# Performance work log

Hardware: AMD Instinct MI355X
Metric: run time of the kernel (lower is better)

The kernel has to match this reference:

```python
import jax, jax.numpy as jnp
import numpy as np

B, N, D, H, C = 4, 1024, 768, 12, 3
Dh = D // H                      # 64
HID = int(D * 4.0 * (2.0 / 3.0)) # 2048 (SwiGLU hidden)
EPS = 1e-5


def layernorm(x, g, b):
    m = jnp.mean(x, axis=-1, keepdims=True)
    v = jnp.mean(jnp.square(x - m), axis=-1, keepdims=True)
    return (x - m) * jax.lax.rsqrt(v + EPS) * g + b


def setup_inputs() -> dict:
    key = jax.random.key(0)
    ks = jax.random.split(key, 8)
    x = jax.random.normal(ks[0], (B, N, D), jnp.float32)
    coords = jax.random.uniform(ks[1], (B, N, C), jnp.float32)
    qkv_w = jax.random.normal(ks[2], (3 * D, D), jnp.float32) * 0.02
    qkv_b = jnp.zeros((3 * D,), jnp.float32)
    rel_w = jax.random.normal(ks[3], (H, C), jnp.float32) * 0.1
    ln1_g = jnp.ones((D,), jnp.float32)
    ln1_b = jnp.zeros((D,), jnp.float32)
    ln2_g = jnp.ones((D,), jnp.float32)
    ln2_b = jnp.zeros((D,), jnp.float32)
    win_w = jax.random.normal(ks[4], (2 * HID, D), jnp.float32) * 0.02
    win_b = jnp.zeros((2 * HID,), jnp.float32)
    wout_w = jax.random.normal(ks[5], (D, HID), jnp.float32) * 0.02
    wout_b = jnp.zeros((D,), jnp.float32)
    return dict(x=x, coords=coords, ln1_g=ln1_g, ln1_b=ln1_b, qkv_w=qkv_w,
                qkv_b=qkv_b, rel_w=rel_w, ln2_g=ln2_g, ln2_b=ln2_b,
                win_w=win_w, win_b=win_b, wout_w=wout_w, wout_b=wout_b)


def reference(x, coords, ln1_g, ln1_b, qkv_w, qkv_b, rel_w, ln2_g, ln2_b,
              win_w, win_b, wout_w, wout_b):
    # --- PatchAttention on norm1(x) ---
    h = layernorm(x, ln1_g, ln1_b)
    qkv = h @ qkv_w.T + qkv_b                    # (B,N,3D)
    q, k, v = jnp.split(qkv, 3, axis=-1)

    def heads(t):  # (B,N,D) -> (B,H,N,Dh)
        return t.reshape(B, N, H, Dh).transpose(0, 2, 1, 3)

    qh, kh, vh = heads(q), heads(k), heads(v)
    scale = 1.0 / np.sqrt(Dh).astype(np.float32)
    scores = jnp.einsum('bhid,bhjd->bhij', qh, kh) * scale
    # coord bias: (coords_i - coords_j) . W_h  ==  p[b,h,i] - p[b,h,j]
    p = jnp.einsum('bnc,hc->bhn', coords, rel_w)  # (B,H,N)
    scores = scores + p[:, :, :, None] - p[:, :, None, :]
    attn = jax.nn.softmax(scores, axis=-1)
    o = jnp.einsum('bhij,bhjd->bhid', attn, vh)   # (B,H,N,Dh)
    o = o.transpose(0, 2, 1, 3).reshape(B, N, D)
    x = x + o

    # --- SwiGLU FFN on norm2(x) ---
    h2 = layernorm(x, ln2_g, ln2_b)
    uv = h2 @ win_w.T + win_b                     # (B,N,2*HID)
    u, g = jnp.split(uv, 2, axis=-1)
    act = jax.nn.silu(u) * g
    return x + act @ wout_w.T + wout_b
```

## Files before the change

### kernel.cpp

```cpp
#include <hip/hip_runtime.h>
#include <math.h>

typedef unsigned short u16;
typedef __bf16 bf16x8 __attribute__((ext_vector_type(8)));
typedef __bf16 bf16x4 __attribute__((ext_vector_type(4)));
typedef u16 u16x4 __attribute__((ext_vector_type(4)));
typedef float f32x4 __attribute__((ext_vector_type(4)));

#define NTOK 1024
#define DMODEL 768
#define NHEAD 12
#define LD3 2304
#define HIDDIM 2048

__device__ __forceinline__ float b2f(u16 u) {
  unsigned int t = ((unsigned int)u) << 16;
  float f;
  __builtin_memcpy(&f, &t, 4);
  return f;
}
__device__ __forceinline__ u16 f2b(float f) {
  unsigned int t;
  __builtin_memcpy(&t, &f, 4);
  t += 0x7fffu + ((t >> 16) & 1u);
  return (u16)(t >> 16);
}

__device__ __forceinline__ void gl_lds16(const u16* g, u16* l) {
  __builtin_amdgcn_global_load_lds(
      (__attribute__((address_space(1))) const unsigned int*)g,
      (__attribute__((address_space(3))) unsigned int*)l, 16, 0, 0);
}

__global__ __launch_bounds__(256) void signal_kernel(float* __restrict__ out,
                                                     int n, float c) {
  int i = blockIdx.x * 256 + threadIdx.x;
  if (i < n) out[i] = c;
}

struct CanonJobs {
  const void* s[13];
  u16* d[13];
  int n[13];
};

__global__ __launch_bounds__(256) void canon_kernel(CanonJobs jobs) {
  __shared__ int csh;
  u16 v = ((const u16*)jobs.s[0])[2 * threadIdx.x];
  int e = (v >> 7) & 0xFF;
  unsigned long long m = __ballot(e >= 0xC0);
  if (threadIdx.x == 0) csh = 0;
  __syncthreads();
  if ((threadIdx.x & 63) == 0) atomicAdd(&csh, __popcll(m));
  __syncthreads();
  bool isf32 = csh >= 8;

  int j = blockIdx.y;
  int n4 = jobs.n[j] >> 2;
  const void* s = jobs.s[j];
  u16* d = jobs.d[j];
  for (int i = blockIdx.x * 256 + threadIdx.x; i < n4; i += gridDim.x * 256) {
    if (isf32) {
      f32x4 vv = *((const f32x4*)s + i);
      u16x4 o = {f2b(vv[0]), f2b(vv[1]), f2b(vv[2]), f2b(vv[3])};
      *((u16x4*)d + i) = o;
    } else {
      *((u16x4*)d + i) = *((const u16x4*)s + i);
    }
  }
}

__global__ __launch_bounds__(256) void ln_bf16_kernel(
    const u16* __restrict__ x, const u16* __restrict__ g,
    const u16* __restrict__ b, u16* __restrict__ out) {
  int row = blockIdx.x;
  int tid = threadIdx.x;
  const u16* xr = x + (size_t)row * DMODEL;
  float v0 = b2f(xr[tid]), v1 = b2f(xr[tid + 256]), v2 = b2f(xr[tid + 512]);
  float s = v0 + v1 + v2;
  float q = v0 * v0 + v1 * v1 + v2 * v2;
#pragma unroll
  for (int off = 32; off; off >>= 1) {
    s += __shfl_xor(s, off, 64);
    q += __shfl_xor(q, off, 64);
  }
  __shared__ float rs[4], rq[4];
  int wv = tid >> 6;
  if ((tid & 63) == 0) { rs[wv] = s; rq[wv] = q; }
  __syncthreads();
  s = rs[0] + rs[1] + rs[2] + rs[3];
  q = rq[0] + rq[1] + rq[2] + rq[3];
  float mean = s * (1.0f / 768.0f);
  float var = q * (1.0f / 768.0f) - mean * mean;
  float inv = rsqrtf(var + 1e-5f);
  u16* outr = out + (size_t)row * DMODEL;
  outr[tid]       = f2b((v0 - mean) * inv * b2f(g[tid])       + b2f(b[tid]));
  outr[tid + 256] = f2b((v1 - mean) * inv * b2f(g[tid + 256]) + b2f(b[tid + 256]));
  outr[tid + 512] = f2b((v2 - mean) * inv * b2f(g[tid + 512]) + b2f(b[tid + 512]));
}

__global__ __launch_bounds__(256) void ln_f32_kernel(
    const float* __restrict__ x, const u16* __restrict__ g,
    const u16* __restrict__ b, u16* __restrict__ out) {
  int row = blockIdx.x;
  int tid = threadIdx.x;
  const float* xr = x + (size_t)row * DMODEL;
  float v0 = xr[tid], v1 = xr[tid + 256], v2 = xr[tid + 512];
  float s = v0 + v1 + v2;
  float q = v0 * v0 + v1 * v1 + v2 * v2;
#pragma unroll
  for (int off = 32; off; off >>= 1) {
    s += __shfl_xor(s, off, 64);
    q += __shfl_xor(q, off, 64);
  }
  __shared__ float rs[4], rq[4];
  int wv = tid >> 6;
  if ((tid & 63) == 0) { rs[wv] = s; rq[wv] = q; }
  __syncthreads();
  s = rs[0] + rs[1] + rs[2] + rs[3];
  q = rq[0] + rq[1] + rq[2] + rq[3];
  float mean = s * (1.0f / 768.0f);
  float var = q * (1.0f / 768.0f) - mean * mean;
  float inv = rsqrtf(var + 1e-5f);
  u16* outr = out + (size_t)row * DMODEL;
  outr[tid]       = f2b((v0 - mean) * inv * b2f(g[tid])       + b2f(b[tid]));
  outr[tid + 256] = f2b((v1 - mean) * inv * b2f(g[tid + 256]) + b2f(b[tid + 256]));
  outr[tid + 512] = f2b((v2 - mean) * inv * b2f(g[tid + 512]) + b2f(b[tid + 512]));
}

__global__ __launch_bounds__(256) void gemm_bt(
    const u16* __restrict__ Ap, const u16* __restrict__ Wp,
    const u16* __restrict__ bias, u16* __restrict__ Cp, int Nn, int K) {
  __shared__ __align__(16) u16 Al[3 * 128 * 32], Bl[3 * 64 * 32];
  int lane = threadIdx.x & 63;
  int wv = threadIdx.x >> 6;
  int q16 = lane & 15, quad = lane >> 4;
  int mB0 = blockIdx.y * 128;
  int nB0 = blockIdx.x * 64;
  int mW = (wv >> 1) * 64, nW = (wv & 1) * 32;
  int srow = lane >> 2;
  int scol = ((lane & 3) ^ ((lane >> 3) & 3)) * 8;
  int sx8 = (quad ^ ((q16 >> 1) & 3)) * 8;
  int r0 = wv * 32 + srow, r1 = r0 + 16;
  int rb = wv * 16 + srow;
  const u16* Ag0 = Ap + (size_t)(mB0 + r0) * K + scol;
  const u16* Ag1 = Ap + (size_t)(mB0 + r1) * K + scol;
  const u16* Wg  = Wp + (size_t)(nB0 + rb) * K + scol;
  int ch0 = wv * 1024, ch1 = ch0 + 512, chb = wv * 512;
  int nsteps = K >> 5;
  f32x4 acc[4][2] = {};
#pragma unroll
  for (int tt = 0; tt < 2; ++tt) {
    int k0 = tt * 32;
    gl_lds16(Ag0 + k0, Al + tt * 4096 + ch0);
    gl_lds16(Ag1 + k0, Al + tt * 4096 + ch1);
    gl_lds16(Wg + k0, Bl + tt * 2048 + chb);
  }
  int n3 = nsteps / 3;
  for (int kb = 0; kb < n3; ++kb) {
#pragma unroll
    for (int c = 0; c < 3; ++c) {
      int t = kb * 3 + c;
      if (t < nsteps - 1) asm volatile("s_waitcnt vmcnt(3)" ::: "memory");
      else                asm volatile("s_waitcnt vmcnt(0)" ::: "memory");
      __builtin_amdgcn_sched_barrier(0);
      __builtin_amdgcn_s_barrier();
      __builtin_amdgcn_sched_barrier(0);
      if (t < nsteps - 2) {
        int k0 = (t + 2) * 32;
        int bs = (c + 2) % 3;
        gl_lds16(Ag0 + k0, Al + bs * 4096 + ch0);
        gl_lds16(Ag1 + k0, Al + bs * 4096 + ch1);
        gl_lds16(Wg + k0, Bl + bs * 2048 + chb);
      }
      const __bf16* Ab = (const __bf16*)(Al + c * 4096);
      const __bf16* Bb = (const __bf16*)(Bl + c * 2048);
      bf16x8 af[4], bfr[2];
#pragma unroll
      for (int si = 0; si < 4; ++si)
        af[si] = *(const bf16x8*)(Ab + (mW + si * 16 + q16) * 32 + sx8);
#pragma unroll
      for (int sj = 0; sj < 2; ++sj)
        bfr[sj] = *(const bf16x8*)(Bb + (nW + sj * 16 + q16) * 32 + sx8);
#pragma unroll
      for (int si = 0; si < 4; ++si)
#pragma unroll
        for (int sj = 0; sj < 2; ++sj)
          acc[si][sj] = __builtin_amdgcn_mfma_f32_16x16x32_bf16(af[si], bfr[sj], acc[si][sj], 0, 0, 0);
    }
  }
#pragma unroll
  for (int si = 0; si < 4; ++si)
#pragma unroll
    for (int sj = 0; sj < 2; ++sj) {
      int col = nB0 + nW + sj * 16 + q16;
      float bcol = b2f(bias[col]);
#pragma unroll
      for (int r = 0; r < 4; ++r) {
        int rowi = mB0 + mW + si * 16 + quad * 4 + r;
        Cp[(size_t)rowi * Nn + col] = f2b(acc[si][sj][r] + bcol);
      }
    }
}

__global__ __launch_bounds__(256) void gemm_out_f32(
    const u16* __restrict__ Ap, const u16* __restrict__ Wp,
    const u16* __restrict__ bias, const float* __restrict__ res,
    float* __restrict__ out) {
  __shared__ __align__(16) u16 Al[2 * 4096], Bl[2 * 4096];
  int lane = threadIdx.x & 63;
  int wv = threadIdx.x >> 6;
  int q16 = lane & 15, quad = lane >> 4;
  int mB0 = blockIdx.y * 64;
  int nB0 = blockIdx.x * 64;
  int mW = (wv >> 1) * 32, nW = (wv & 1) * 32;
  int lr = lane >> 3, ls = lane & 7;
  int sg = (ls ^ lr) * 8;
  int sx0 = (quad ^ (q16 & 7)) * 8;
  int sx1 = ((4 | quad) ^ (q16 & 7)) * 8;
  const u16* Ag = Ap + (size_t)(mB0 + wv * 16 + lr) * 2048 + sg;
  const u16* Wg = Wp + (size_t)(nB0 + wv * 16 + lr) * 2048 + sg;
  int ch = wv * 1024;
  f32x4 acc[2][2] = {};
#pragma unroll
  for (int i = 0; i < 2; ++i) {
    gl_lds16(Ag + (size_t)i * 8 * 2048, Al + ch + i * 512);
    gl_lds16(Wg + (size_t)i * 8 * 2048, Bl + ch + i * 512);
  }
  for (int kb = 0; kb < 16; ++kb) {
#pragma unroll
    for (int c = 0; c < 2; ++c) {
      int t = kb * 2 + c;
      asm volatile("s_waitcnt vmcnt(0)" ::: "memory");
      __builtin_amdgcn_sched_barrier(0);
      __builtin_amdgcn_s_barrier();
      __builtin_amdgcn_sched_barrier(0);
      if (t < 31) {
        int k0 = (t + 1) * 64;
        int bs = c ^ 1;
#pragma unroll
        for (int i = 0; i < 2; ++i) {
          gl_lds16(Ag + (size_t)i * 8 * 2048 + k0, Al + bs * 4096 + ch + i * 512);
          gl_lds16(Wg + (size_t)i * 8 * 2048 + k0, Bl + bs * 4096 + ch + i * 512);
        }
      }
      const __bf16* Ab = (const __bf16*)(Al + c * 4096);
      const __bf16* Bb = (const __bf16*)(Bl + c * 4096);
      bf16x8 a0[2], a1[2], b0[2], b1[2];
#pragma unroll
      for (int si = 0; si < 2; ++si) {
        a0[si] = *(const bf16x8*)(Ab + (mW + si * 16 + q16) * 64 + sx0);
        a1[si] = *(const bf16x8*)(Ab + (mW + si * 16 + q16) * 64 + sx1);
      }
#pragma unroll
      for (int sj = 0; sj < 2; ++sj) {
        b0[sj] = *(const bf16x8*)(Bb + (nW + sj * 16 + q16) * 64 + sx0);
        b1[sj] = *(const bf16x8*)(Bb + (nW + sj * 16 + q16) * 64 + sx1);
      }
#pragma unroll
      for (int si = 0; si < 2; ++si)
#pragma unroll
        for (int sj = 0; sj < 2; ++sj) {
          acc[si][sj] = __builtin_amdgcn_mfma_f32_16x16x32_bf16(a0[si], b0[sj], acc[si][sj], 0, 0, 0);
          acc[si][sj] = __builtin_amdgcn_mfma_f32_16x16x32_bf16(a1[si], b1[sj], acc[si][sj], 0, 0, 0);
        }
    }
  }
#pragma unroll
  for (int si = 0; si < 2; ++si)
#pragma unroll
    for (int sj = 0; sj < 2; ++sj) {
      int col = nB0 + nW + sj * 16 + q16;
      float bcol = b2f(bias[col]);
#pragma unroll
      for (int r = 0; r < 4; ++r) {
        int rowi = mB0 + mW + si * 16 + quad * 4 + r;
        size_t idx = (size_t)rowi * 768 + col;
        out[idx] = acc[si][sj][r] + bcol + res[idx];
      }
    }
}

__global__ __launch_bounds__(256) void ffn_in_kernel(
    const u16* __restrict__ hp, const u16* __restrict__ Wp,
    const u16* __restrict__ bias, u16* __restrict__ actp) {
  __shared__ __align__(16) u16 Al[2 * 8192], Bl[2 * 4096];
  int lane = threadIdx.x & 63;
  int wv = threadIdx.x >> 6;
  int q16 = lane & 15, quad = lane >> 4;
  int mB0 = blockIdx.y * 128;
  int cB0 = blockIdx.x * 32;
  int mW = (wv >> 1) * 64;
  int cW = (wv & 1) * 16;
  int lr = lane >> 3, ls = lane & 7;
  int sg = (ls ^ lr) * 8;
  int sx0 = (quad ^ (q16 & 7)) * 8;
  int sx1 = ((4 | quad) ^ (q16 & 7)) * 8;
  const u16* Ag = hp + (size_t)(mB0 + wv * 32 + lr) * DMODEL + sg;
  int rB0 = wv * 16 + lr, rB1 = rB0 + 8;
  int gb0 = (rB0 < 32) ? (cB0 + rB0) : (HIDDIM + cB0 + rB0 - 32);
  int gb1 = (rB1 < 32) ? (cB0 + rB1) : (HIDDIM + cB0 + rB1 - 32);
  const u16* Wg0 = Wp + (size_t)gb0 * DMODEL + sg;
  const u16* Wg1 = Wp + (size_t)gb1 * DMODEL + sg;
  int chA = wv * 2048, chB = wv * 1024;
  f32x4 au[4] = {}, ag[4] = {};
#pragma unroll
  for (int i = 0; i < 4; ++i)
    gl_lds16(Ag + (size_t)i * 8 * DMODEL, Al + chA + i * 512);
  gl_lds16(Wg0, Bl + chB);
  gl_lds16(Wg1, Bl + chB + 512);
  for (int kb = 0; kb < 6; ++kb) {
#pragma unroll
    for (int c = 0; c < 2; ++c) {
      int t = kb * 2 + c;
      asm volatile("s_waitcnt vmcnt(0)" ::: "memory");
      __builtin_amdgcn_sched_barrier(0);
      __builtin_amdgcn_s_barrier();
      __builtin_amdgcn_sched_barrier(0);
      if (t < 11) {
        int k0 = (t + 1) * 64;
        int bs = c ^ 1;
#pragma unroll
        for (int i = 0; i < 4; ++i)
          gl_lds16(Ag + (size_t)i * 8 * DMODEL + k0, Al + bs * 8192 + chA + i * 512);
        gl_lds16(Wg0 + k0, Bl + bs * 4096 + chB);
        gl_lds16(Wg1 + k0, Bl + bs * 4096 + chB + 512);
      }
      const __bf16* Ab = (const __bf16*)(Al + c * 8192);
      const __bf16* Bb = (const __bf16*)(Bl + c * 4096);
      bf16x8 a0[4], a1[4];
#pragma unroll
      for (int si = 0; si < 4; ++si) {
        a0[si] = *(const bf16x8*)(Ab + (mW + si * 16 + q16) * 64 + sx0);
        a1[si] = *(const bf16x8*)(Ab + (mW + si * 16 + q16) * 64 + sx1);
      }
      bf16x8 wu0 = *(const bf16x8*)(Bb + (cW + q16) * 64 + sx0);
      bf16x8 wu1 = *(const bf16x8*)(Bb + (cW + q16) * 64 + sx1);
      bf16x8 wg0 = *(const bf16x8*)(Bb + (32 + cW + q16) * 64 + sx0);
      bf16x8 wg1 = *(const bf16x8*)(Bb + (32 + cW + q16) * 64 + sx1);
#pragma unroll
      for (int si = 0; si < 4; ++si) {
        au[si] = __builtin_amdgcn_mfma_f32_16x16x32_bf16(a0[si], wu0, au[si], 0, 0, 0);
        ag[si] = __builtin_amdgcn_mfma_f32_16x16x32_bf16(a0[si], wg0, ag[si], 0, 0, 0);
      }
#pragma unroll
      for (int si = 0; si < 4; ++si) {
        au[si] = __builtin_amdgcn_mfma_f32_16x16x32_bf16(a1[si], wu1, au[si], 0, 0, 0);
        ag[si] = __builtin_amdgcn_mfma_f32_16x16x32_bf16(a1[si], wg1, ag[si], 0, 0, 0);
      }
    }
  }
  int col = cB0 + cW + q16;
  float bu = b2f(bias[col]);
  float bg = b2f(bias[HIDDIM + col]);
#pragma unroll
  for (int si = 0; si < 4; ++si) {
#pragma unroll
    for (int r = 0; r < 4; ++r) {
      int rowi = mB0 + mW + si * 16 + quad * 4 + r;
      float u = au[si][r] + bu;
      float g = ag[si][r] + bg;
      float s = u / (1.0f + __expf(-u));
      actp[(size_t)rowi * HIDDIM + col] = f2b(s * g);
    }
  }
}

__global__ __launch_bounds__(256) void vt_kernel(const u16* __restrict__ qkvp,
                                                 u16* __restrict__ vtp,
                                                 const u16* __restrict__ coords,
                                                 const u16* __restrict__ relw,
                                                 float* __restrict__ p) {
  int blk = blockIdx.x;
  int b = blk / 192;
  int rem = blk % 192;
  int h = rem >> 4;
  int nt = rem & 15;
  int wv = threadIdx.x >> 6;
  int d = threadIdx.x & 63;
  int n0 = nt * 64 + wv * 16;
  const u16* src = qkvp + ((size_t)(b * NTOK) + n0) * LD3 + 2 * DMODEL + h * 64 + d;
  u16* dst = vtp + ((size_t)((b * NHEAD + h) * 64 + d)) * NTOK + n0;
#pragma unroll
  for (int c = 0; c < 2; ++c) {
    u16 buf[8] __attribute__((aligned(16)));
#pragma unroll
    for (int i = 0; i < 8; ++i) buf[i] = src[(size_t)(c * 8 + i) * LD3];
    *(uint4*)(dst + c * 8) = *(const uint4*)buf;
  }
  if (nt == 0) {
    const float LOG2E = 1.4426950408889634f;
    float w0 = b2f(relw[h * 3 + 0]), w1 = b2f(relw[h * 3 + 1]), w2 = b2f(relw[h * 3 + 2]);
    float* prow = p + (size_t)(b * NHEAD + h) * NTOK;
    for (int n = threadIdx.x; n < NTOK; n += 256) {
      int idx = b * NTOK + n;
      float c0 = b2f(coords[idx * 3 + 0]);
      float c1 = b2f(coords[idx * 3 + 1]);
      float c2 = b2f(coords[idx * 3 + 2]);
      prow[n] = (c0 * w0 + c1 * w1 + c2 * w2) * LOG2E;
    }
  }
}

__global__ __launch_bounds__(256) void attn_kernel(
    const u16* __restrict__ qkvp, const u16* __restrict__ vtp,
    const float* __restrict__ p2, const u16* __restrict__ xp,
    float* __restrict__ x1) {
  const __bf16* qb = (const __bf16*)qkvp;
  __shared__ __align__(16) u16 Kl[2][64 * 64];
  __shared__ __align__(16) u16 Vl[2][64 * 64];
  __shared__ __align__(16) u16 Pl[4][16][64];
  __shared__ __align__(16) float Pb[1024];
  int lane = threadIdx.x & 63;
  int wv = threadIdx.x >> 6;
  int hw = blockIdx.x;
  int g = hw % 48;
  int nt = hw / 48;
  int b = g / 12, h = g % 12;
  int i0 = (nt * 4 + wv) * 16;
  int q16 = lane & 15, quad = lane >> 4;

  const float scl2 = 0.125f * 1.4426950408889634f;

  const __bf16* qrow = qb + ((size_t)(b * NTOK) + i0 + q16) * LD3 + h * 64;
  bf16x8 bq0 = *(const bf16x8*)(qrow + quad * 8);
  bf16x8 bq1 = *(const bf16x8*)(qrow + 32 + quad * 8);

  const float* prow = p2 + (size_t)(b * NHEAD + h) * NTOK;

  int lr = lane >> 3, ls = lane & 7;
  int krw = wv * 16 + lr;
  int ksl = ls ^ (krw & 7);
  const u16* kg0 = qkvp + (size_t)(b * NTOK) * LD3 + DMODEL + h * 64 + ksl * 8;
  const u16* vg0 = vtp + ((size_t)((b * NHEAD + h) * 64 + krw)) * NTOK + ksl * 8;

  int kx0 = (quad ^ (q16 & 7)) << 3;
  int kx1 = ((4 | quad) ^ (q16 & 7)) << 3;

  float mrun = -1e30f, lsum = 0.f;
  f32x4 accO[4] = {};

  gl_lds16((const u16*)(prow + wv * 256 + lane * 4), (u16*)&Pb[wv * 256]);
  gl_lds16(kg0 + (size_t)krw * LD3, &Kl[0][wv * 1024]);
  gl_lds16(kg0 + (size_t)(krw + 8) * LD3, &Kl[0][wv * 1024 + 512]);
  gl_lds16(vg0, &Vl[0][wv * 1024]);
  gl_lds16(vg0 + (size_t)8 * NTOK, &Vl[0][wv * 1024 + 512]);

  for (int t = 0; t < 16; ++t) {
    asm volatile("s_waitcnt vmcnt(0)" ::: "memory");
    __builtin_amdgcn_sched_barrier(0);
    __builtin_amdgcn_s_barrier();
    __builtin_amdgcn_sched_barrier(0);
    int c = t & 1;
    if (t < 15) {
      int j = (t + 1) * 64;
      int bs = c ^ 1;
      gl_lds16(kg0 + (size_t)(j + krw) * LD3, &Kl[bs][wv * 1024]);
      gl_lds16(kg0 + (size_t)(j + krw + 8) * LD3, &Kl[bs][wv * 1024 + 512]);
      gl_lds16(vg0 + j, &Vl[bs][wv * 1024]);
      gl_lds16(vg0 + (size_t)8 * NTOK + j, &Vl[bs][wv * 1024 + 512]);
    }

    int j0 = t * 64;
    const __bf16* Kb = (const __bf16*)Kl[c];
    const __bf16* Vb = (const __bf16*)Vl[c];

    f32x4 st[4];
#pragma unroll
    for (int tt = 0; tt < 4; ++tt) {
      bf16x8 ka0 = *(const bf16x8*)(Kb + (tt * 16 + q16) * 64 + kx0);
      bf16x8 ka1 = *(const bf16x8*)(Kb + (tt * 16 + q16) * 64 + kx1);
      f32x4 z = {};
      z = __builtin_amdgcn_mfma_f32_16x16x32_bf16(ka0, bq0, z, 0, 0, 0);
      z = __builtin_amdgcn_mfma_f32_16x16x32_bf16(ka1, bq1, z, 0, 0, 0);
      st[tt] = z;
    }

    float sv[4][4];
#pragma unroll
    for (int tt = 0; tt < 4; ++tt) {
      f32x4 pj = *(const f32x4*)(&Pb[j0 + tt * 16 + 4 * quad]);
#pragma unroll
      for (int r = 0; r < 4; ++r) sv[tt][r] = st[tt][r] * scl2 - pj[r];
    }
    float lm = sv[0][0];
#pragma unroll
    for (int tt = 0; tt < 4; ++tt)
#pragma unroll
      for (int r = 0; r < 4; ++r) lm = fmaxf(lm, sv[tt][r]);
    lm = fmaxf(lm, __shfl_xor(lm, 16, 64));
    lm = fmaxf(lm, __shfl_xor(lm, 32, 64));
    float mn = fmaxf(mrun, lm);
    float alpha = exp2f(mrun - mn);
    mrun = mn;
    float pp[4][4];
    float ts = 0.f;
#pragma unroll
    for (int tt = 0; tt < 4; ++tt) {
      float s0 = exp2f(sv[tt][0] - mn), s1 = exp2f(sv[tt][1] - mn);
      float s2 = exp2f(sv[tt][2] - mn), s3 = exp2f(sv[tt][3] - mn);
      pp[tt][0] = s0; pp[tt][1] = s1; pp[tt][2] = s2; pp[tt][3] = s3;
      ts += (s0 + s1) + (s2 + s3);
    }
    ts += __shfl_xor(ts, 16, 64);
    ts += __shfl_xor(ts, 32, 64);
    lsum = lsum * alpha + ts;

#pragma unroll
    for (int tt = 0; tt < 4; ++tt) {
      bf16x4 w = {(__bf16)pp[tt][0], (__bf16)pp[tt][1],
                  (__bf16)pp[tt][2], (__bf16)pp[tt][3]};
      int wslot = (2 * tt + (quad >> 1)) ^ (q16 & 7);
      *(bf16x4*)(&Pl[wv][q16][wslot * 8 + (quad & 1) * 4]) = w;
    }
    bf16x8 ap0 = *(const bf16x8*)(&Pl[wv][q16][kx0]);
    bf16x8 ap1 = *(const bf16x8*)(&Pl[wv][q16][kx1]);

#pragma unroll
    for (int ds = 0; ds < 4; ++ds) {
      bf16x8 av0 = *(const bf16x8*)(Vb + (ds * 16 + q16) * 64 + kx0);
      bf16x8 av1 = *(const bf16x8*)(Vb + (ds * 16 + q16) * 64 + kx1);
      f32x4 cc = accO[ds];
#pragma unroll
      for (int r = 0; r < 4; ++r) cc[r] *= alpha;
      cc = __builtin_amdgcn_mfma_f32_16x16x32_bf16(av0, ap0, cc, 0, 0, 0);
      cc = __builtin_amdgcn_mfma_f32_16x16x32_bf16(av1, ap1, cc, 0, 0, 0);
      accO[ds] = cc;
    }
  }

  float rl = 1.0f / lsum;
  size_t rowbase = ((size_t)(b * NTOK) + i0 + q16) * DMODEL + h * 64;
#pragma unroll
  for (int ds = 0; ds < 4; ++ds) {
    int d0 = ds * 16 + quad * 4;
    u16x4 xv = *(const u16x4*)(xp + rowbase + d0);
    f32x4 ov;
#pragma unroll
    for (int r = 0; r < 4; ++r) ov[r] = b2f(xv[r]) + accO[ds][r] * rl;
    *(f32x4*)(x1 + rowbase + d0) = ov;
  }
}

extern "C" void kernel_launch(void* const* d_in, const int* in_sizes, int n_in,
                              void* d_out, int out_size, void* d_ws, size_t ws_size,
                              hipStream_t stream) {
  static const int esz[13] = {3145728, 12288, 768, 768, 1769472, 2304, 36,
                              768, 768, 3145728, 4096, 1572864, 768};
  float sig = -1.f;
  if (n_in != 13) {
    sig = 6000.f + 100.f * (float)n_in;
  } else {
    for (int i = 0; i < 13; ++i)
      if (in_sizes[i] != esz[i]) { sig = 1000.f + 100.f * (float)i; break; }
  }
  if (sig < 0.f && ws_size < 57258496ULL) sig = 3000.f;
  if (sig < 0.f && out_size != 3145728) sig = 3100.f;
  if (sig >= 0.f) {
    signal_kernel<<<(out_size + 255) / 256, 256, 0, stream>>>((float*)d_out, out_size, sig);
    return;
  }

  char* ws = (char*)d_ws;
  u16*  cx      = (u16*)(ws + 256);
  u16*  cqkvw   = (u16*)(ws + 6291712);
  u16*  cwinw   = (u16*)(ws + 9830656);
  u16*  cwoutw  = (u16*)(ws + 16122112);
  u16*  ccoords = (u16*)(ws + 19267840);
  u16*  cln1g   = (u16*)(ws + 19292416);
  u16*  cln1b   = (u16*)(ws + 19293952);
  u16*  cqkvb   = (u16*)(ws + 19295488);
  u16*  crelw   = (u16*)(ws + 19300096);
  u16*  cln2g   = (u16*)(ws + 19300352);
  u16*  cln2b   = (u16*)(ws + 19301888);
  u16*  cwinb   = (u16*)(ws + 19303424);
  u16*  cwoutb  = (u16*)(ws + 19311616);
  u16*  h       = (u16*)(ws + 19313152);
  u16*  qkv     = (u16*)(ws + 25604608);
  float* pbuf   = (float*)(ws + 44478976);
  float* x1     = (float*)(ws + 44675584);
  u16*  act     = qkv;
  u16*  vt      = h;

  CanonJobs jobs;
  u16* dsts[13] = {cx, ccoords, cln1g, cln1b, cqkvw, cqkvb, crelw,
                   cln2g, cln2b, cwinw, cwinb, cwoutw, cwoutb};
  for (int i = 0; i < 13; ++i) {
    jobs.s[i] = d_in[i];
    jobs.d[i] = dsts[i];
    jobs.n[i] = in_sizes[i];
  }
  canon_kernel<<<dim3(768, 13), 256, 0, stream>>>(jobs);

  ln_bf16_kernel<<<4096, 256, 0, stream>>>(cx, cln1g, cln1b, h);
  gemm_bt<<<dim3(36, 32), 256, 0, stream>>>(h, cqkvw, cqkvb, qkv, 2304, 768);
  vt_kernel<<<768, 256, 0, stream>>>(qkv, vt, ccoords, crelw, pbuf);
  attn_kernel<<<768, 256, 0, stream>>>(qkv, vt, pbuf, cx, x1);
  ln_f32_kernel<<<4096, 256, 0, stream>>>(x1, cln2g, cln2b, h);
  ffn_in_kernel<<<dim3(64, 32), 256, 0, stream>>>(h, cwinw, cwinb, act);
  gemm_out_f32<<<dim3(12, 64), 256, 0, stream>>>(act, cwoutw, cwoutb, x1,
                                                 (float*)d_out);
}
```

Baseline: 265.4 us.

## Fuse V transpose into QKV GEMM epilogue and widen FFN-in tiles

The QKV GEMM epilogue now writes Q/K into a 1536-wide buffer and writes V directly in transposed per-head layout. This removes the separate vt_kernel and one full pass over V. The coordinate-bias projection moves into the first LayerNorm kernel. The FFN input kernel is retiled to 64 hidden columns per block with doubled LDS for weights, giving more MFMA reuse per A tile but fewer blocks and higher register and LDS use.

Result: faster. 257.2 us (-3.1%).

```diff
diff --git a/kernel.cpp b/kernel.cpp
--- a/kernel.cpp
+++ b/kernel.cpp
@@ -10,7 +10,7 @@
 #define NTOK 1024
 #define DMODEL 768
 #define NHEAD 12
-#define LD3 2304
+#define LD2 1536
 #define HIDDIM 2048
 
 __device__ __forceinline__ float b2f(u16 u) {
@@ -72,7 +72,9 @@
 
 __global__ __launch_bounds__(256) void ln_bf16_kernel(
     const u16* __restrict__ x, const u16* __restrict__ g,
-    const u16* __restrict__ b, u16* __restrict__ out) {
+    const u16* __restrict__ b, u16* __restrict__ out,
+    const u16* __restrict__ coords, const u16* __restrict__ relw,
+    float* __restrict__ p) {
   int row = blockIdx.x;
   int tid = threadIdx.x;
   const u16* xr = x + (size_t)row * DMODEL;
@@ -97,6 +99,19 @@
   outr[tid]       = f2b((v0 - mean) * inv * b2f(g[tid])       + b2f(b[tid]));
   outr[tid + 256] = f2b((v1 - mean) * inv * b2f(g[tid + 256]) + b2f(b[tid + 256]));
   outr[tid + 512] = f2b((v2 - mean) * inv * b2f(g[tid + 512]) + b2f(b[tid + 512]));
+  if (row < 48) {
+    const float LOG2E = 1.4426950408889634f;
+    int bb = row / 12, hh = row % 12;
+    float w0 = b2f(relw[hh * 3 + 0]), w1 = b2f(relw[hh * 3 + 1]), w2 = b2f(relw[hh * 3 + 2]);
+    float* prow = p + (size_t)(bb * NHEAD + hh) * NTOK;
+    for (int n = tid; n < NTOK; n += 256) {
+      int idx = bb * NTOK + n;
+      float c0 = b2f(coords[idx * 3 + 0]);
+      float c1 = b2f(coords[idx * 3 + 1]);
+      float c2 = b2f(coords[idx * 3 + 2]);
+      prow[n] = (c0 * w0 + c1 * w1 + c2 * w2) * LOG2E;
+    }
+  }
 }
 
 __global__ __launch_bounds__(256) void ln_f32_kernel(
@@ -130,7 +145,8 @@
 
 __global__ __launch_bounds__(256) void gemm_bt(
     const u16* __restrict__ Ap, const u16* __restrict__ Wp,
-    const u16* __restrict__ bias, u16* __restrict__ Cp, int Nn, int K) {
+    const u16* __restrict__ bias, u16* __restrict__ Cp,
+    u16* __restrict__ vtp, int K) {
   __shared__ __align__(16) u16 Al[3 * 128 * 32], Bl[3 * 64 * 32];
   int lane = threadIdx.x & 63;
   int wv = threadIdx.x >> 6;
@@ -189,18 +205,35 @@
           acc[si][sj] = __builtin_amdgcn_mfma_f32_16x16x32_bf16(af[si], bfr[sj], acc[si][sj], 0, 0, 0);
     }
   }
-#pragma unroll
-  for (int si = 0; si < 4; ++si)
-#pragma unroll
-    for (int sj = 0; sj < 2; ++sj) {
-      int col = nB0 + nW + sj * 16 + q16;
-      float bcol = b2f(bias[col]);
-#pragma unroll
-      for (int r = 0; r < 4; ++r) {
-        int rowi = mB0 + mW + si * 16 + quad * 4 + r;
-        Cp[(size_t)rowi * Nn + col] = f2b(acc[si][sj][r] + bcol);
-      }
-    }
+  if (nB0 < 1536) {
+#pragma unroll
+    for (int si = 0; si < 4; ++si)
+#pragma unroll
+      for (int sj = 0; sj < 2; ++sj) {
+        int col = nB0 + nW + sj * 16 + q16;
+        float bcol = b2f(bias[col]);
+#pragma unroll
+        for (int r = 0; r < 4; ++r) {
+          int rowi = mB0 + mW + si * 16 + quad * 4 + r;
+          Cp[(size_t)rowi * LD2 + col] = f2b(acc[si][sj][r] + bcol);
+        }
+      }
+  } else {
+#pragma unroll
+    for (int si = 0; si < 4; ++si)
+#pragma unroll
+      for (int sj = 0; sj < 2; ++sj) {
+        int col = nB0 + nW + sj * 16 + q16;
+        float bcol = b2f(bias[col]);
+        int vd = col - 1536;
+        int hh = vd >> 6, dd = vd & 63;
+        int n0 = mB0 + mW + si * 16 + quad * 4;
+        int bb = n0 >> 10, nn = n0 & 1023;
+        u16x4 o = {f2b(acc[si][sj][0] + bcol), f2b(acc[si][sj][1] + bcol),
+                   f2b(acc[si][sj][2] + bcol), f2b(acc[si][sj][3] + bcol)};
+        *(u16x4*)(vtp + ((size_t)((bb * NHEAD + hh) * 64 + dd)) * NTOK + nn) = o;
+      }
+  }
 }
 
 __global__ __launch_bounds__(256) void gemm_out_f32(
@@ -284,31 +317,33 @@
 __global__ __launch_bounds__(256) void ffn_in_kernel(
     const u16* __restrict__ hp, const u16* __restrict__ Wp,
     const u16* __restrict__ bias, u16* __restrict__ actp) {
-  __shared__ __align__(16) u16 Al[2 * 8192], Bl[2 * 4096];
+  __shared__ __align__(16) u16 Al[2 * 8192], Bl[2 * 8192];
   int lane = threadIdx.x & 63;
   int wv = threadIdx.x >> 6;
   int q16 = lane & 15, quad = lane >> 4;
   int mB0 = blockIdx.y * 128;
-  int cB0 = blockIdx.x * 32;
+  int cB0 = blockIdx.x * 64;
   int mW = (wv >> 1) * 64;
-  int cW = (wv & 1) * 16;
+  int cW = (wv & 1) * 32;
   int lr = lane >> 3, ls = lane & 7;
   int sg = (ls ^ lr) * 8;
   int sx0 = (quad ^ (q16 & 7)) * 8;
   int sx1 = ((4 | quad) ^ (q16 & 7)) * 8;
   const u16* Ag = hp + (size_t)(mB0 + wv * 32 + lr) * DMODEL + sg;
-  int rB0 = wv * 16 + lr, rB1 = rB0 + 8;
-  int gb0 = (rB0 < 32) ? (cB0 + rB0) : (HIDDIM + cB0 + rB0 - 32);
-  int gb1 = (rB1 < 32) ? (cB0 + rB1) : (HIDDIM + cB0 + rB1 - 32);
-  const u16* Wg0 = Wp + (size_t)gb0 * DMODEL + sg;
-  const u16* Wg1 = Wp + (size_t)gb1 * DMODEL + sg;
-  int chA = wv * 2048, chB = wv * 1024;
-  f32x4 au[4] = {}, ag[4] = {};
-#pragma unroll
-  for (int i = 0; i < 4; ++i)
+  const u16* Wgp[4];
+#pragma unroll
+  for (int i = 0; i < 4; ++i) {
+    int rbb = wv * 32 + i * 8 + lr;
+    int gb = (rbb < 64) ? (cB0 + rbb) : (HIDDIM + cB0 + rbb - 64);
+    Wgp[i] = Wp + (size_t)gb * DMODEL + sg;
+  }
+  int chA = wv * 2048, chB = wv * 2048;
+  f32x4 au[4][2] = {}, ag[4][2] = {};
+#pragma unroll
+  for (int i = 0; i < 4; ++i) {
     gl_lds16(Ag + (size_t)i * 8 * DMODEL, Al + chA + i * 512);
-  gl_lds16(Wg0, Bl + chB);
-  gl_lds16(Wg1, Bl + chB + 512);
+    gl_lds16(Wgp[i], Bl + chB + i * 512);
+  }
   for (int kb = 0; kb < 6; ++kb) {
 #pragma unroll
     for (int c = 0; c < 2; ++c) {
@@ -321,85 +356,54 @@
         int k0 = (t + 1) * 64;
         int bs = c ^ 1;
 #pragma unroll
-        for (int i = 0; i < 4; ++i)
+        for (int i = 0; i < 4; ++i) {
           gl_lds16(Ag + (size_t)i * 8 * DMODEL + k0, Al + bs * 8192 + chA + i * 512);
-        gl_lds16(Wg0 + k0, Bl + bs * 4096 + chB);
-        gl_lds16(Wg1 + k0, Bl + bs * 4096 + chB + 512);
+          gl_lds16(Wgp[i] + k0, Bl + bs * 8192 + chB + i * 512);
+        }
       }
       const __bf16* Ab = (const __bf16*)(Al + c * 8192);
-      const __bf16* Bb = (const __bf16*)(Bl + c * 4096);
+      const __bf16* Bb = (const __bf16*)(Bl + c * 8192);
       bf16x8 a0[4], a1[4];
 #pragma unroll
       for (int si = 0; si < 4; ++si) {
         a0[si] = *(const bf16x8*)(Ab + (mW + si * 16 + q16) * 64 + sx0);
         a1[si] = *(const bf16x8*)(Ab + (mW + si * 16 + q16) * 64 + sx1);
       }
-      bf16x8 wu0 = *(const bf16x8*)(Bb + (cW + q16) * 64 + sx0);
-      bf16x8 wu1 = *(const bf16x8*)(Bb + (cW + q16) * 64 + sx1);
-      bf16x8 wg0 = *(const bf16x8*)(Bb + (32 + cW + q16) * 64 + sx0);
-      bf16x8 wg1 = *(const bf16x8*)(Bb + (32 + cW + q16) * 64 + sx1);
-#pragma unroll
-      for (int si = 0; si < 4; ++si) {
-        au[si] = __builtin_amdgcn_mfma_f32_16x16x32_bf16(a0[si], wu0, au[si], 0, 0, 0);
-        ag[si] = __builtin_amdgcn_mfma_f32_16x16x32_bf16(a0[si], wg0, ag[si], 0, 0, 0);
-      }
-#pragma unroll
-      for (int si = 0; si < 4; ++si) {
-        au[si] = __builtin_amdgcn_mfma_f32_16x16x32_bf16(a1[si], wu1, au[si], 0, 0, 0);
-        ag[si] = __builtin_amdgcn_mfma_f32_16x16x32_bf16(a1[si], wg1, ag[si], 0, 0, 0);
-      }
-    }
-  }
-  int col = cB0 + cW + q16;
-  float bu = b2f(bias[col]);
-  float bg = b2f(bias[HIDDIM + col]);
-#pragma unroll
-  for (int si = 0; si < 4; ++si) {
-#pragma unroll
-    for (int r = 0; r < 4; ++r) {
-      int rowi = mB0 + mW + si * 16 + quad * 4 + r;
-      float u = au[si][r] + bu;
-      float g = ag[si][r] + bg;
-      float s = u / (1.0f + __expf(-u));
-      actp[(size_t)rowi * HIDDIM + col] = f2b(s * g);
-    }
-  }
-}
-
-__global__ __launch_bounds__(256) void vt_kernel(const u16* __restrict__ qkvp,
-                                                 u16* __restrict__ vtp,
-                                                 const u16* __restrict__ coords,
-                                                 const u16* __restrict__ relw,
-                                                 float* __restrict__ p) {
-  int blk = blockIdx.x;
-  int b = blk / 192;
-  int rem = blk % 192;
-  int h = rem >> 4;
-  int nt = rem & 15;
-  int wv = threadIdx.x >> 6;
-  int d = threadIdx.x & 63;
-  int n0 = nt * 64 + wv * 16;
-  const u16* src = qkvp + ((size_t)(b * NTOK) + n0) * LD3 + 2 * DMODEL + h * 64 + d;
-  u16* dst = vtp + ((size_t)((b * NHEAD + h) * 64 + d)) * NTOK + n0;
-#pragma unroll
-  for (int c = 0; c < 2; ++c) {
-    u16 buf[8] __attribute__((aligned(16)));
-#pragma unroll
-    for (int i = 0; i < 8; ++i) buf[i] = src[(size_t)(c * 8 + i) * LD3];
-    *(uint4*)(dst + c * 8) = *(const uint4*)buf;
-  }
-  if (nt == 0) {
-    const float LOG2E = 1.4426950408889634f;
-    float w0 = b2f(relw[h * 3 + 0]), w1 = b2f(relw[h * 3 + 1]), w2 = b2f(relw[h * 3 + 2]);
-    float* prow = p + (size_t)(b * NHEAD + h) * NTOK;
-    for (int n = threadIdx.x; n < NTOK; n += 256) {
-      int idx = b * NTOK + n;
-      float c0 = b2f(coords[idx * 3 + 0]);
-      float c1 = b2f(coords[idx * 3 + 1]);
-      float c2 = b2f(coords[idx * 3 + 2]);
-      prow[n] = (c0 * w0 + c1 * w1 + c2 * w2) * LOG2E;
-    }
-  }
+      bf16x8 wu0[2], wu1[2], wg0[2], wg1[2];
+#pragma unroll
+      for (int sj = 0; sj < 2; ++sj) {
+        wu0[sj] = *(const bf16x8*)(Bb + (cW + sj * 16 + q16) * 64 + sx0);
+        wu1[sj] = *(const bf16x8*)(Bb + (cW + sj * 16 + q16) * 64 + sx1);
+        wg0[sj] = *(const bf16x8*)(Bb + (64 + cW + sj * 16 + q16) * 64 + sx0);
+        wg1[sj] = *(const bf16x8*)(Bb + (64 + cW + sj * 16 + q16) * 64 + sx1);
+      }
+#pragma unroll
+      for (int si = 0; si < 4; ++si)
+#pragma unroll
+        for (int sj = 0; sj < 2; ++sj) {
+          au[si][sj] = __builtin_amdgcn_mfma_f32_16x16x32_bf16(a0[si], wu0[sj], au[si][sj], 0, 0, 0);
+          au[si][sj] = __builtin_amdgcn_mfma_f32_16x16x32_bf16(a1[si], wu1[sj], au[si][sj], 0, 0, 0);
+          ag[si][sj] = __builtin_amdgcn_mfma_f32_16x16x32_bf16(a0[si], wg0[sj], ag[si][sj], 0, 0, 0);
+          ag[si][sj] = __builtin_amdgcn_mfma_f32_16x16x32_bf16(a1[si], wg1[sj], ag[si][sj], 0, 0, 0);
+        }
+    }
+  }
+#pragma unroll
+  for (int si = 0; si < 4; ++si)
+#pragma unroll
+    for (int sj = 0; sj < 2; ++sj) {
+      int col = cB0 + cW + sj * 16 + q16;
+      float bu = b2f(bias[col]);
+      float bg = b2f(bias[HIDDIM + col]);
+#pragma unroll
+      for (int r = 0; r < 4; ++r) {
+        int rowi = mB0 + mW + si * 16 + quad * 4 + r;
+        float u = au[si][sj][r] + bu;
+        float g = ag[si][sj][r] + bg;
+        float s = u / (1.0f + __expf(-u));
+        actp[(size_t)rowi * HIDDIM + col] = f2b(s * g);
+      }
+    }
 }
 
 __global__ __launch_bounds__(256) void attn_kernel(
@@ -422,7 +426,7 @@
 
   const float scl2 = 0.125f * 1.4426950408889634f;
 
-  const __bf16* qrow = qb + ((size_t)(b * NTOK) + i0 + q16) * LD3 + h * 64;
+  const __bf16* qrow = qb + ((size_t)(b * NTOK) + i0 + q16) * LD2 + h * 64;
   bf16x8 bq0 = *(const bf16x8*)(qrow + quad * 8);
   bf16x8 bq1 = *(const bf16x8*)(qrow + 32 + quad * 8);
 
@@ -431,7 +435,7 @@
   int lr = lane >> 3, ls = lane & 7;
   int krw = wv * 16 + lr;
   int ksl = ls ^ (krw & 7);
-  const u16* kg0 = qkvp + (size_t)(b * NTOK) * LD3 + DMODEL + h * 64 + ksl * 8;
+  const u16* kg0 = qkvp + (size_t)(b * NTOK) * LD2 + DMODEL + h * 64 + ksl * 8;
   const u16* vg0 = vtp + ((size_t)((b * NHEAD + h) * 64 + krw)) * NTOK + ksl * 8;
 
   int kx0 = (quad ^ (q16 & 7)) << 3;
@@ -441,8 +445,8 @@
   f32x4 accO[4] = {};
 
   gl_lds16((const u16*)(prow + wv * 256 + lane * 4), (u16*)&Pb[wv * 256]);
-  gl_lds16(kg0 + (size_t)krw * LD3, &Kl[0][wv * 1024]);
-  gl_lds16(kg0 + (size_t)(krw + 8) * LD3, &Kl[0][wv * 1024 + 512]);
+  gl_lds16(kg0 + (size_t)krw * LD2, &Kl[0][wv * 1024]);
+  gl_lds16(kg0 + (size_t)(krw + 8) * LD2, &Kl[0][wv * 1024 + 512]);
   gl_lds16(vg0, &Vl[0][wv * 1024]);
   gl_lds16(vg0 + (size_t)8 * NTOK, &Vl[0][wv * 1024 + 512]);
 
@@ -455,8 +459,8 @@
     if (t < 15) {
       int j = (t + 1) * 64;
       int bs = c ^ 1;
-      gl_lds16(kg0 + (size_t)(j + krw) * LD3, &Kl[bs][wv * 1024]);
-      gl_lds16(kg0 + (size_t)(j + krw + 8) * LD3, &Kl[bs][wv * 1024 + 512]);
+      gl_lds16(kg0 + (size_t)(j + krw) * LD2, &Kl[bs][wv * 1024]);
+      gl_lds16(kg0 + (size_t)(j + krw + 8) * LD2, &Kl[bs][wv * 1024 + 512]);
       gl_lds16(vg0 + j, &Vl[bs][wv * 1024]);
       gl_lds16(vg0 + (size_t)8 * NTOK + j, &Vl[bs][wv * 1024 + 512]);
     }
@@ -576,11 +580,11 @@
   u16*  cwinb   = (u16*)(ws + 19303424);
   u16*  cwoutb  = (u16*)(ws + 19311616);
   u16*  h       = (u16*)(ws + 19313152);
-  u16*  qkv     = (u16*)(ws + 25604608);
+  u16*  qkv2    = (u16*)(ws + 25604608);
+  u16*  vt      = (u16*)(ws + 38187520);
   float* pbuf   = (float*)(ws + 44478976);
   float* x1     = (float*)(ws + 44675584);
-  u16*  act     = qkv;
-  u16*  vt      = h;
+  u16*  act     = qkv2;
 
   CanonJobs jobs;
   u16* dsts[13] = {cx, ccoords, cln1g, cln1b, cqkvw, cqkvb, crelw,
@@ -592,12 +596,12 @@
   }
   canon_kernel<<<dim3(768, 13), 256, 0, stream>>>(jobs);
 
-  ln_bf16_kernel<<<4096, 256, 0, stream>>>(cx, cln1g, cln1b, h);
-  gemm_bt<<<dim3(36, 32), 256, 0, stream>>>(h, cqkvw, cqkvb, qkv, 2304, 768);
-  vt_kernel<<<768, 256, 0, stream>>>(qkv, vt, ccoords, crelw, pbuf);
-  attn_kernel<<<768, 256, 0, stream>>>(qkv, vt, pbuf, cx, x1);
+  ln_bf16_kernel<<<4096, 256, 0, stream>>>(cx, cln1g, cln1b, h,
+                                           ccoords, crelw, pbuf);
+  gemm_bt<<<dim3(36, 32), 256, 0, stream>>>(h, cqkvw, cqkvb, qkv2, vt, 768);
+  attn_kernel<<<768, 256, 0, stream>>>(qkv2, vt, pbuf, cx, x1);
   ln_f32_kernel<<<4096, 256, 0, stream>>>(x1, cln2g, cln2b, h);
-  ffn_in_kernel<<<dim3(64, 32), 256, 0, stream>>>(h, cwinw, cwinb, act);
+  ffn_in_kernel<<<dim3(32, 32), 256, 0, stream>>>(h, cwinw, cwinb, act);
   gemm_out_f32<<<dim3(12, 64), 256, 0, stream>>>(act, cwoutw, cwoutb, x1,
                                                  (float*)d_out);
 }
```
